# Optimization experiments

Measured on AMD Instinct MI355X. Metric: run time of the kernel, lower is better.

## Reference

```python
import jax, jax.numpy as jnp
import numpy as np

N = 10000      # nodes
E = 160000     # edges (before self-loops)
F_IN = 128     # num_features
H1, D1 = 4, 256   # conv1: 4 heads x 256, concat -> 1024
D2 = 256          # conv2: 1 head x 256
NEG_SLOPE = 0.2


def setup_inputs() -> dict:
    key = jax.random.key(0)
    ks = jax.random.split(key, 12)
    def p(k, shape, fan):
        return jax.random.normal(k, shape, jnp.float32) / np.float32(np.sqrt(fan))
    return {
        "x": jax.random.normal(ks[0], (N, F_IN), jnp.float32),
        "edge_index": jax.random.randint(ks[1], (2, E), 0, N, jnp.int32),
        "W1": p(ks[2], (F_IN, H1 * D1), F_IN),
        "att_src1": p(ks[3], (H1, D1), D1),
        "att_dst1": p(ks[4], (H1, D1), D1),
        "b1": jnp.zeros((H1 * D1,), jnp.float32),
        "lin1_W": p(ks[5], (F_IN, H1 * D1), F_IN),
        "lin1_b": jnp.zeros((H1 * D1,), jnp.float32),
        "W2": p(ks[6], (H1 * D1, D2), H1 * D1),
        "att_src2": p(ks[7], (1, D2), D2),
        "att_dst2": p(ks[8], (1, D2), D2),
        "b2": jnp.zeros((D2,), jnp.float32),
        "lin2_W": p(ks[9], (H1 * D1, D2), H1 * D1),
        "lin2_b": jnp.zeros((D2,), jnp.float32),
    }


def gat_layer(x, src, dst, W, a_src, a_dst, b, heads, d):
    """PyG-style GATConv: transform, edgewise LeakyReLU attention,
    segment-softmax over destination neighborhoods, scatter-add, concat heads."""
    n = x.shape[0]
    h = (x @ W).reshape(n, heads, d)                       # [N, H, D]
    s_src = jnp.einsum('nhd,hd->nh', h, a_src)             # per-node scores
    s_dst = jnp.einsum('nhd,hd->nh', h, a_dst)
    e = jax.nn.leaky_relu(s_src[src] + s_dst[dst], NEG_SLOPE)   # [E, H]
    m = jax.ops.segment_max(e, dst, num_segments=n)        # stable softmax per dst
    p = jnp.exp(e - m[dst])
    z = jax.ops.segment_sum(p, dst, num_segments=n)
    alpha = p / (z[dst] + 1e-16)                           # [E, H]
    msg = h[src] * alpha[:, :, None]                       # [E, H, D]
    out = jax.ops.segment_sum(msg, dst, num_segments=n)    # [N, H, D]
    return out.reshape(n, heads * d) + b, alpha


def reference(x, edge_index, W1, att_src1, att_dst1, b1, lin1_W, lin1_b,
              W2, att_src2, att_dst2, b2, lin2_W, lin2_b):
    n = x.shape[0]
    loop = jnp.arange(n, dtype=edge_index.dtype)           # add self-loops (PyG default)
    src = jnp.concatenate([edge_index[0], loop])
    dst = jnp.concatenate([edge_index[1], loop])
    h1, alpha1 = gat_layer(x, src, dst, W1, att_src1, att_dst1, b1, H1, D1)
    h1 = jax.nn.elu(h1 + x @ lin1_W + lin1_b)              # conv1 + lin1 residual, ELU
    h2, _ = gat_layer(h1, src, dst, W2, att_src2, att_dst2, b2, 1, D2)
    out = h2 + h1 @ lin2_W + lin2_b                        # conv2 + lin2 residual
    return out, alpha1
```

## Files before the change

kernel.cpp:

```cpp
#include <hip/hip_runtime.h>
#include <hip/hip_bf16.h>
#include <math.h>

#define NN   10000
#define EE   160000
#define ETOT 170000
#define FIN  128
#define C1   1024
#define NH1  4
#define D1   256
#define D2   256
#define MAXD 96

typedef __attribute__((ext_vector_type(8))) short bf16x8;
typedef __attribute__((ext_vector_type(4))) float f32x4;

__device__ __forceinline__ float b2f(unsigned short u)
{
    union { unsigned int i; float f; } c; c.i = (unsigned int)u << 16; return c.f;
}
__device__ __forceinline__ unsigned short f2b(float x)
{
    return __builtin_bit_cast(unsigned short, __float2bfloat16(x));
}
__device__ __forceinline__ void split1(float x, unsigned short &h, unsigned short &l)
{
    __hip_bfloat16 hb = __float2bfloat16(x);
    float r = x - __bfloat162float(hb);
    h = __builtin_bit_cast(unsigned short, hb);
    l = __builtin_bit_cast(unsigned short, __float2bfloat16(r));
}

__global__ __launch_bounds__(256)
void split_A(const float* __restrict__ X, unsigned short* __restrict__ A2, int M, int K)
{
    int idx = blockIdx.x * 256 + threadIdx.x;
    int kq4 = K >> 2;
    if (idx >= M * kq4) return;
    int m = idx / kq4, kq = idx % kq4;
    float4 v = *(const float4*)&X[(size_t)m * K + kq * 4];
    ushort4 h, l;
    split1(v.x, h.x, l.x); split1(v.y, h.y, l.y);
    split1(v.z, h.z, l.z); split1(v.w, h.w, l.w);
    unsigned short* row = A2 + (size_t)m * (2 * K);
    *(ushort4*)&row[kq * 4]     = h;
    *(ushort4*)&row[K + kq * 4] = l;
}

__global__ __launch_bounds__(256)
void split_Bt(const float* __restrict__ B0, const float* __restrict__ B1,
              int K, int N0, int Ntot, unsigned short* __restrict__ Bt)
{
    int idx = blockIdx.x * 256 + threadIdx.x;
    int total = Ntot * (K >> 2);
    if (idx >= total) return;
    int n = idx % Ntot;
    int kq = idx / Ntot;
    int k = kq * 4;
    const float* B; int nc, nb;
    if (n < N0) { B = B0; nc = n; nb = N0; }
    else        { B = B1; nc = n - N0; nb = Ntot - N0; }
    float v0 = B[(size_t)(k + 0) * nb + nc];
    float v1 = B[(size_t)(k + 1) * nb + nc];
    float v2 = B[(size_t)(k + 2) * nb + nc];
    float v3 = B[(size_t)(k + 3) * nb + nc];
    ushort4 h, l;
    split1(v0, h.x, l.x); split1(v1, h.y, l.y);
    split1(v2, h.z, l.z); split1(v3, h.w, l.w);
    unsigned short* row = Bt + (size_t)n * (3 * K);
    *(ushort4*)&row[k]         = h;
    *(ushort4*)&row[K + k]     = h;
    *(ushort4*)&row[2 * K + k] = l;
}

__device__ __forceinline__ void glds16(const void* g, void* l)
{
    __builtin_amdgcn_global_load_lds((const __attribute__((address_space(1))) void*)g,
                                     (__attribute__((address_space(3))) void*)l, 16, 0, 0);
}

template<int BN, int WM, int WN, int BK>
__global__ __launch_bounds__(256)
void gemm_split(const unsigned short* __restrict__ A, int lda, int ka2,
                const unsigned short* __restrict__ Bt, int keff,
                unsigned short* __restrict__ outPb, float* __restrict__ outR,
                int M, int nsplit, int ldR, int ntn,
                const float* __restrict__ bias0, const float* __restrict__ bias1)
{
    constexpr int BM   = 128;
    constexpr int WTM  = BM / WM,  WTN = BN / WN;
    constexpr int FJ   = WTM / 16, FI  = WTN / 16;
    constexpr int KS   = BK / 32;
    constexpr int SLOTS = BK / 8;
    constexpr int SMASK = SLOTS - 1;
    constexpr int SWSH  = (BK == 32) ? 1 : 0;
    constexpr int RPC  = 512 / BK;
    constexpr int ACH  = BM / RPC;
    constexpr int NCH  = (BM + BN) / RPC;
    constexpr int CPW  = NCH / 4;
    constexpr int ABUF = BM * BK, BBUF = BN * BK;

    __shared__ __align__(16) unsigned short sA[2 * ABUF];
    __shared__ __align__(16) unsigned short sB[2 * BBUF];

    const int tid = threadIdx.x;
    const int w = tid >> 6, lane = tid & 63;

    const int cpx = gridDim.x >> 3;
    const int t0  = (blockIdx.x & 7) * cpx + (blockIdx.x >> 3);
    const int m0 = (t0 / ntn) * BM;
    const int n0 = (t0 % ntn) * BN;
    const int wm = w / WN, wn = w % WN;

    f32x4 acc[FI][FJ] = {};

    const unsigned short* gp[CPW];
    int lofs[CPW];
    bool isa[CPW];
    {
        const int r  = lane / SLOTS;
        const int sl = lane % SLOTS;
        const int ssl = sl ^ ((r >> SWSH) & SMASK);
        #pragma unroll
        for (int cc = 0; cc < CPW; ++cc) {
            int c = w * CPW + cc;
            if (c < ACH) {
                int gm = m0 + c * RPC + r; if (gm >= M) gm = M - 1;
                gp[cc]   = A + (size_t)gm * lda + ssl * 8;
                lofs[cc] = c * 512;
                isa[cc]  = true;
            } else {
                int gn = n0 + (c - ACH) * RPC + r;
                gp[cc]   = Bt + (size_t)gn * keff + ssl * 8;
                lofs[cc] = (c - ACH) * 512;
                isa[cc]  = false;
            }
        }
    }

    const int rAl = wm * WTM + (lane & 15);
    const int rBl = wn * WTN + (lane & 15);
    const int koff = (lane >> 4) * 8;
    const int nit = keff / BK;
    int cur = 0;

    #pragma unroll
    for (int cc = 0; cc < CPW; ++cc)
        glds16(gp[cc], (isa[cc] ? sA : sB) + lofs[cc]);
    __syncthreads();

    for (int it = 0; it < nit; ++it) {
        if (it + 1 < nit) {
            int kn = (it + 1) * BK;
            int kAn = (kn >= ka2) ? (kn - ka2) : kn;
            #pragma unroll
            for (int cc = 0; cc < CPW; ++cc) {
                unsigned short* dst = (isa[cc] ? sA + (cur ^ 1) * ABUF
                                               : sB + (cur ^ 1) * BBUF) + lofs[cc];
                glds16(gp[cc] + (isa[cc] ? kAn : kn), dst);
            }
        }
        const unsigned short* cA = sA + cur * ABUF;
        const unsigned short* cB = sB + cur * BBUF;
        #pragma unroll
        for (int ks = 0; ks < KS; ++ks) {
            const int sIdx = (ks * 32 + koff) >> 3;
            bf16x8 av[FJ], bv[FI];
            #pragma unroll
            for (int f = 0; f < FI; ++f) {
                int row = rBl + f * 16;
                bv[f] = *(const bf16x8*)&cB[row * BK + ((sIdx ^ ((row >> SWSH) & SMASK)) << 3)];
            }
            #pragma unroll
            for (int f = 0; f < FJ; ++f) {
                int row = rAl + f * 16;
                av[f] = *(const bf16x8*)&cA[row * BK + ((sIdx ^ ((row >> SWSH) & SMASK)) << 3)];
            }
            #pragma unroll
            for (int fj = 0; fj < FJ; ++fj)
                #pragma unroll
                for (int fi = 0; fi < FI; ++fi)
                    acc[fi][fj] = __builtin_amdgcn_mfma_f32_16x16x32_bf16(
                        bv[fi], av[fj], acc[fi][fj], 0, 0, 0);
        }
        __syncthreads();
        cur ^= 1;
    }

    const int lrow = lane & 15;
    const int lcol = (lane >> 4) << 2;
    #pragma unroll
    for (int fj = 0; fj < FJ; ++fj) {
        int row = m0 + wm * WTM + fj * 16 + lrow;
        if (row >= M) continue;
        #pragma unroll
        for (int fi = 0; fi < FI; ++fi) {
            int col = n0 + wn * WTN + fi * 16 + lcol;
            f32x4 v = acc[fi][fj];
            if (col < nsplit) {
                ushort4 o;
                o.x = f2b(v[0]); o.y = f2b(v[1]); o.z = f2b(v[2]); o.w = f2b(v[3]);
                *(ushort4*)&outPb[(size_t)row * nsplit + col] = o;
            } else {
                int c = col - nsplit;
                const float4 g0 = *(const float4*)&bias0[c];
                const float4 g1 = *(const float4*)&bias1[c];
                v[0] += g0.x + g1.x; v[1] += g0.y + g1.y;
                v[2] += g0.z + g1.z; v[3] += g0.w + g1.w;
                *(f32x4*)&outR[(size_t)row * ldR + c] = v;
            }
        }
    }
}

__global__ __launch_bounds__(256)
void scores_h4(const unsigned short* __restrict__ h, const float* __restrict__ a_src,
               const float* __restrict__ a_dst, float* __restrict__ s_src,
               float* __restrict__ s_dst)
{
    const int n = blockIdx.x;
    const int w = threadIdx.x >> 6;
    const int lane = threadIdx.x & 63;
    ushort4 u = *(const ushort4*)&h[(size_t)n * C1 + w * D1 + lane * 4];
    float4 as = ((const float4*)&a_src[w * D1])[lane];
    float4 ad = ((const float4*)&a_dst[w * D1])[lane];
    float vx = b2f(u.x), vy = b2f(u.y), vz = b2f(u.z), vw = b2f(u.w);
    float ss = vx * as.x + vy * as.y + vz * as.z + vw * as.w;
    float sd = vx * ad.x + vy * ad.y + vz * ad.z + vw * ad.w;
    #pragma unroll
    for (int off = 32; off; off >>= 1) {
        ss += __shfl_xor(ss, off);
        sd += __shfl_xor(sd, off);
    }
    if (lane == 0) { s_src[n * NH1 + w] = ss; s_dst[n * NH1 + w] = sd; }
}

__global__ __launch_bounds__(256)
void scores_h1(const unsigned short* __restrict__ h, const float* __restrict__ a_src,
               const float* __restrict__ a_dst, float* __restrict__ s_src,
               float* __restrict__ s_dst)
{
    const int n = blockIdx.x * 4 + (threadIdx.x >> 6);
    if (n >= NN) return;
    const int lane = threadIdx.x & 63;
    ushort4 u = *(const ushort4*)&h[(size_t)n * D2 + lane * 4];
    float4 as = ((const float4*)a_src)[lane];
    float4 ad = ((const float4*)a_dst)[lane];
    float vx = b2f(u.x), vy = b2f(u.y), vz = b2f(u.z), vw = b2f(u.w);
    float ss = vx * as.x + vy * as.y + vz * as.z + vw * as.w;
    float sd = vx * ad.x + vy * ad.y + vz * ad.z + vw * ad.w;
    #pragma unroll
    for (int off = 32; off; off >>= 1) {
        ss += __shfl_xor(ss, off);
        sd += __shfl_xor(sd, off);
    }
    if (lane == 0) { s_src[n] = ss; s_dst[n] = sd; }
}

__global__ void count_deg(const int* __restrict__ dstp, int* __restrict__ cnt)
{
    int e = blockIdx.x * 256 + threadIdx.x;
    if (e >= ETOT) return;
    int d = (e < EE) ? dstp[e] : (e - EE);
    atomicAdd(&cnt[d], 1);
}

__global__ __launch_bounds__(1024)
void scan_kernel(const int* __restrict__ cnt, int* __restrict__ row_ptr)
{
    __shared__ int part[1024];
    const int t = threadIdx.x;
    int local[10];
    int s = 0;
    #pragma unroll
    for (int j = 0; j < 10; ++j) {
        int idx = t * 10 + j;
        local[j] = s;
        s += (idx < NN) ? cnt[idx] : 0;
    }
    part[t] = s;
    __syncthreads();
    for (int off = 1; off < 1024; off <<= 1) {
        int v = (t >= off) ? part[t - off] : 0;
        __syncthreads();
        part[t] += v;
        __syncthreads();
    }
    int prefix = (t > 0) ? part[t - 1] : 0;
    #pragma unroll
    for (int j = 0; j < 10; ++j) {
        int idx = t * 10 + j;
        if (idx < NN) row_ptr[idx] = prefix + local[j];
    }
    if (t == 0) row_ptr[NN] = ETOT;
}

__global__ void scatter_edges(const int* __restrict__ srcp, const int* __restrict__ dstp,
                              const int* __restrict__ row_ptr, int* __restrict__ fill,
                              int* __restrict__ csr_src, int* __restrict__ csr_eid)
{
    int e = blockIdx.x * 256 + threadIdx.x;
    if (e >= ETOT) return;
    int s, d;
    if (e < EE) { s = srcp[e]; d = dstp[e]; } else { s = d = e - EE; }
    int pos = row_ptr[d] + atomicAdd(&fill[d], 1);
    csr_src[pos] = s;
    csr_eid[pos] = e;
}

__global__ __launch_bounds__(256)
void aggregate1(const unsigned short* __restrict__ h1b, const float* __restrict__ s_src,
                const float* __restrict__ s_dst,
                const int* __restrict__ row_ptr, const int* __restrict__ csr_src,
                const int* __restrict__ csr_eid, const float* __restrict__ base_in,
                unsigned short* __restrict__ a2stk, float* __restrict__ alpha_out)
{
    __shared__ float lalpha[NH1][MAXD];
    const int n = blockIdx.x;
    const int t = threadIdx.x;
    const int h = t >> 6;
    const int lane = t & 63;
    const int start = row_ptr[n], end = row_ptr[n + 1];
    const float sd = s_dst[n * NH1 + h];

    float m = -1e30f;
    for (int i = start + lane; i < end; i += 64) {
        float sc = s_src[csr_src[i] * NH1 + h] + sd;
        sc = sc > 0.f ? sc : 0.2f * sc;
        m = fmaxf(m, sc);
    }
    #pragma unroll
    for (int off = 32; off; off >>= 1) m = fmaxf(m, __shfl_xor(m, off));
    float z = 0.f;
    for (int i = start + lane; i < end; i += 64) {
        float sc = s_src[csr_src[i] * NH1 + h] + sd;
        sc = sc > 0.f ? sc : 0.2f * sc;
        z += __expf(sc - m);
    }
    #pragma unroll
    for (int off = 32; off; off >>= 1) z += __shfl_xor(z, off);
    const float invz = 1.f / (z + 1e-16f);
    for (int i = start + lane; i < end; i += 64) {
        float sc = s_src[csr_src[i] * NH1 + h] + sd;
        sc = sc > 0.f ? sc : 0.2f * sc;
        float a = __expf(sc - m) * invz;
        alpha_out[(size_t)csr_eid[i] * NH1 + h] = a;
        int idx = i - start;
        if (idx < MAXD) lalpha[h][idx] = a;
    }
    __syncthreads();

    float4 base = *(const float4*)&base_in[(size_t)n * C1 + t * 4];
    float4 acc = make_float4(0.f, 0.f, 0.f, 0.f);
    for (int i = start; i < end; ++i) {
        const int s = csr_src[i];
        const int idx = i - start;
        float a;
        if (idx < MAXD) {
            a = lalpha[h][idx];
        } else {
            float sc = s_src[s * NH1 + h] + sd;
            sc = sc > 0.f ? sc : 0.2f * sc;
            a = __expf(sc - m) * invz;
        }
        ushort4 v = *(const ushort4*)&h1b[(size_t)s * C1 + t * 4];
        acc.x += a * b2f(v.x); acc.y += a * b2f(v.y);
        acc.z += a * b2f(v.z); acc.w += a * b2f(v.w);
    }
    float4 r;
    r.x = acc.x + base.x; r.y = acc.y + base.y;
    r.z = acc.z + base.z; r.w = acc.w + base.w;
    r.x = r.x > 0.f ? r.x : expm1f(r.x);
    r.y = r.y > 0.f ? r.y : expm1f(r.y);
    r.z = r.z > 0.f ? r.z : expm1f(r.z);
    r.w = r.w > 0.f ? r.w : expm1f(r.w);
    __syncthreads();
    ushort4 hi, lo;
    split1(r.x, hi.x, lo.x); split1(r.y, hi.y, lo.y);
    split1(r.z, hi.z, lo.z); split1(r.w, hi.w, lo.w);
    unsigned short* row = a2stk + (size_t)n * (2 * C1);
    *(ushort4*)&row[t * 4]      = hi;
    *(ushort4*)&row[C1 + t * 4] = lo;
}

__global__ __launch_bounds__(64)
void aggregate2(const unsigned short* __restrict__ h2b, const float* __restrict__ s_src,
                const float* __restrict__ s_dst,
                const int* __restrict__ row_ptr, const int* __restrict__ csr_src,
                const float* __restrict__ accin, float* __restrict__ out)
{
    __shared__ float lalpha[MAXD];
    const int n = blockIdx.x;
    const int t = threadIdx.x;
    const int start = row_ptr[n], end = row_ptr[n + 1];
    const float sd = s_dst[n];

    float m = -1e30f;
    for (int i = start + t; i < end; i += 64) {
        float sc = s_src[csr_src[i]] + sd;
        sc = sc > 0.f ? sc : 0.2f * sc;
        m = fmaxf(m, sc);
    }
    #pragma unroll
    for (int off = 32; off; off >>= 1) m = fmaxf(m, __shfl_xor(m, off));
    float z = 0.f;
    for (int i = start + t; i < end; i += 64) {
        float sc = s_src[csr_src[i]] + sd;
        sc = sc > 0.f ? sc : 0.2f * sc;
        z += __expf(sc - m);
    }
    #pragma unroll
    for (int off = 32; off; off >>= 1) z += __shfl_xor(z, off);
    const float invz = 1.f / (z + 1e-16f);
    for (int i = start + t; i < end; i += 64) {
        float sc = s_src[csr_src[i]] + sd;
        sc = sc > 0.f ? sc : 0.2f * sc;
        int idx = i - start;
        if (idx < MAXD) lalpha[idx] = __expf(sc - m) * invz;
    }
    __syncthreads();

    float4 acc = make_float4(0.f, 0.f, 0.f, 0.f);
    for (int i = start; i < end; ++i) {
        const int s = csr_src[i];
        const int idx = i - start;
        float a;
        if (idx < MAXD) {
            a = lalpha[idx];
        } else {
            float sc = s_src[s] + sd;
            sc = sc > 0.f ? sc : 0.2f * sc;
            a = __expf(sc - m) * invz;
        }
        ushort4 v = *(const ushort4*)&h2b[(size_t)s * D2 + t * 4];
        acc.x += a * b2f(v.x); acc.y += a * b2f(v.y);
        acc.z += a * b2f(v.z); acc.w += a * b2f(v.w);
    }
    float4 base = *(const float4*)&accin[(size_t)n * D2 + t * 4];
    float4 r;
    r.x = acc.x + base.x; r.y = acc.y + base.y;
    r.z = acc.z + base.z; r.w = acc.w + base.w;
    *(float4*)&out[(size_t)n * D2 + t * 4] = r;
}

extern "C" void kernel_launch(void* const* d_in, const int* in_sizes, int n_in,
                              void* d_out, int out_size, void* d_ws, size_t ws_size,
                              hipStream_t stream)
{
    const float* x        = (const float*)d_in[0];
    const int*   ei       = (const int*)  d_in[1];
    const float* W1       = (const float*)d_in[2];
    const float* att_src1 = (const float*)d_in[3];
    const float* att_dst1 = (const float*)d_in[4];
    const float* b1       = (const float*)d_in[5];
    const float* lin1_W   = (const float*)d_in[6];
    const float* lin1_b   = (const float*)d_in[7];
    const float* W2       = (const float*)d_in[8];
    const float* att_src2 = (const float*)d_in[9];
    const float* att_dst2 = (const float*)d_in[10];
    const float* b2       = (const float*)d_in[11];
    const float* lin2_W   = (const float*)d_in[12];
    const float* lin2_b   = (const float*)d_in[13];
    const int* srcp = ei;
    const int* dstp = ei + EE;

    float* out    = (float*)d_out;
    float* alpha1 = out + (size_t)NN * D2;

    float* fw = (float*)d_ws;
    float* acc1   = fw;   fw += (size_t)NN * C1;
    unsigned short* h1b = (unsigned short*)fw; fw += (size_t)NN * C1 / 2;
    unsigned short* h2b = (unsigned short*)fw; fw += (size_t)NN * D2 / 2;
    float* acc2   = fw;   fw += (size_t)NN * D2;
    unsigned short* A1stk = (unsigned short*)fw; fw += (size_t)NN * FIN;
    unsigned short* Bt1   = (unsigned short*)fw; fw += (size_t)2048 * 3 * FIN / 2;
    unsigned short* Bt2   = (unsigned short*)fw; fw += (size_t)512 * 3 * C1 / 2;
    float* s_src1 = fw;   fw += NN * NH1;
    float* s_dst1 = fw;   fw += NN * NH1;
    float* s_src2 = fw;   fw += NN;
    float* s_dst2 = fw;   fw += NN;
    int* ip      = (int*)fw;
    int* cnt     = ip;    ip += NN;
    int* fill    = ip;    ip += NN;
    int* row_ptr = ip;    ip += NN + 4;
    int* csr_src = ip;    ip += ETOT;
    int* csr_eid = ip;    ip += ETOT;

    unsigned short* A2stk = (unsigned short*)acc1;

    hipMemsetAsync(cnt, 0, 2 * NN * sizeof(int), stream);

    const int mt = (NN + 127) / 128;

    split_A<<<(NN * (FIN / 4) + 255) / 256, 256, 0, stream>>>(x, A1stk, NN, FIN);
    split_Bt<<<(2048 * (FIN / 4) + 255) / 256, 256, 0, stream>>>(W1, lin1_W, FIN, C1, 2048, Bt1);
    gemm_split<128, 2, 2, 32><<<mt * 16, 256, 0, stream>>>(
        A1stk, 2 * FIN, 2 * FIN, Bt1, 3 * FIN, h1b, acc1, NN, C1, C1, 16, lin1_b, b1);
    scores_h4<<<NN, 256, 0, stream>>>(h1b, att_src1, att_dst1, s_src1, s_dst1);

    count_deg<<<(ETOT + 255) / 256, 256, 0, stream>>>(dstp, cnt);
    scan_kernel<<<1, 1024, 0, stream>>>(cnt, row_ptr);
    scatter_edges<<<(ETOT + 255) / 256, 256, 0, stream>>>(srcp, dstp, row_ptr, fill,
                                                          csr_src, csr_eid);

    aggregate1<<<NN, 256, 0, stream>>>(h1b, s_src1, s_dst1, row_ptr, csr_src, csr_eid,
                                       acc1, A2stk, alpha1);

    split_Bt<<<(512 * (C1 / 4) + 255) / 256, 256, 0, stream>>>(W2, lin2_W, C1, D2, 512, Bt2);
    gemm_split<64, 4, 1, 64><<<mt * 8, 256, 0, stream>>>(
        A2stk, 2 * C1, 2 * C1, Bt2, 3 * C1, h2b, acc2, NN, D2, D2, 8, lin2_b, b2);

    scores_h1<<<(NN + 3) / 4, 256, 0, stream>>>(h2b, att_src2, att_dst2, s_src2, s_dst2);
    aggregate2<<<NN, 64, 0, stream>>>(h2b, s_src2, s_dst2, row_ptr, csr_src, acc2, out);
}
```

Measured before the change: 237.4 us.

## Fuse prep kernels into one launch and sort CSR segments by source

Merges split_A, both split_Bt weight conversions and the degree count into a single prep kernel with block-range dispatch, removing three kernel launches. Adds a sort_segments kernel that bitonic-sorts each destination's neighbor list by (src, eid) within a wavefront, making the atomic-order CSR deterministic and improving gather locality in aggregation. The trade-off is one extra kernel launch and the sort work, and segments with more than 64 neighbors are left unsorted.

```diff
diff --git a/kernel.cpp b/kernel.cpp
--- a/kernel.cpp
+++ b/kernel.cpp
@@ -31,10 +31,10 @@
     l = __builtin_bit_cast(unsigned short, __float2bfloat16(r));
 }
 
-__global__ __launch_bounds__(256)
-void split_A(const float* __restrict__ X, unsigned short* __restrict__ A2, int M, int K)
-{
-    int idx = blockIdx.x * 256 + threadIdx.x;
+__device__ __forceinline__ void split_A_body(const float* __restrict__ X,
+                                             unsigned short* __restrict__ A2,
+                                             int M, int K, int idx)
+{
     int kq4 = K >> 2;
     if (idx >= M * kq4) return;
     int m = idx / kq4, kq = idx % kq4;
@@ -47,11 +47,11 @@
     *(ushort4*)&row[K + kq * 4] = l;
 }
 
-__global__ __launch_bounds__(256)
-void split_Bt(const float* __restrict__ B0, const float* __restrict__ B1,
-              int K, int N0, int Ntot, unsigned short* __restrict__ Bt)
-{
-    int idx = blockIdx.x * 256 + threadIdx.x;
+__device__ __forceinline__ void split_Bt_body(const float* __restrict__ B0,
+                                              const float* __restrict__ B1,
+                                              int K, int N0, int Ntot,
+                                              unsigned short* __restrict__ Bt, int idx)
+{
     int total = Ntot * (K >> 2);
     if (idx >= total) return;
     int n = idx % Ntot;
@@ -71,6 +71,30 @@
     *(ushort4*)&row[k]         = h;
     *(ushort4*)&row[K + k]     = h;
     *(ushort4*)&row[2 * K + k] = l;
+}
+
+__global__ __launch_bounds__(256)
+void prep(const float* __restrict__ x, unsigned short* __restrict__ A1stk,
+          const float* __restrict__ W1, const float* __restrict__ lin1_W,
+          unsigned short* __restrict__ Bt1,
+          const float* __restrict__ W2, const float* __restrict__ lin2_W,
+          unsigned short* __restrict__ Bt2,
+          const int* __restrict__ dstp, int* __restrict__ cnt)
+{
+    const int b = blockIdx.x, t = threadIdx.x;
+    if (b < 1250) {
+        split_A_body(x, A1stk, NN, FIN, b * 256 + t);
+    } else if (b < 1506) {
+        split_Bt_body(W1, lin1_W, FIN, C1, 2048, Bt1, (b - 1250) * 256 + t);
+    } else if (b < 2018) {
+        split_Bt_body(W2, lin2_W, C1, D2, 512, Bt2, (b - 1506) * 256 + t);
+    } else {
+        int e = (b - 2018) * 256 + t;
+        if (e < ETOT) {
+            int d = (e < EE) ? dstp[e] : (e - EE);
+            atomicAdd(&cnt[d], 1);
+        }
+    }
 }
 
 __device__ __forceinline__ void glds16(const void* g, void* l)
@@ -257,14 +281,6 @@
     if (lane == 0) { s_src[n] = ss; s_dst[n] = sd; }
 }
 
-__global__ void count_deg(const int* __restrict__ dstp, int* __restrict__ cnt)
-{
-    int e = blockIdx.x * 256 + threadIdx.x;
-    if (e >= ETOT) return;
-    int d = (e < EE) ? dstp[e] : (e - EE);
-    atomicAdd(&cnt[d], 1);
-}
-
 __global__ __launch_bounds__(1024)
 void scan_kernel(const int* __restrict__ cnt, int* __restrict__ row_ptr)
 {
@@ -306,6 +322,34 @@
     int pos = row_ptr[d] + atomicAdd(&fill[d], 1);
     csr_src[pos] = s;
     csr_eid[pos] = e;
+}
+
+__global__ __launch_bounds__(256)
+void sort_segments(const int* __restrict__ row_ptr, int* __restrict__ csr_src,
+                   int* __restrict__ csr_eid)
+{
+    const int n = blockIdx.x * 4 + (threadIdx.x >> 6);
+    if (n >= NN) return;
+    const int lane = threadIdx.x & 63;
+    const int start = row_ptr[n], end = row_ptr[n + 1];
+    const int deg = end - start;
+    if (deg > 64) return;
+    unsigned int key = 0xFFFFFFFFu;
+    if (lane < deg)
+        key = ((unsigned)csr_src[start + lane] << 18) | (unsigned)csr_eid[start + lane];
+    #pragma unroll
+    for (int k = 2; k <= 64; k <<= 1) {
+        #pragma unroll
+        for (int j = k >> 1; j > 0; j >>= 1) {
+            unsigned int pk = (unsigned int)__shfl_xor((int)key, j);
+            bool wantMin = (((lane & k) == 0) == ((lane & j) == 0));
+            key = wantMin ? (key < pk ? key : pk) : (key > pk ? key : pk);
+        }
+    }
+    if (lane < deg) {
+        csr_src[start + lane] = (int)(key >> 18);
+        csr_eid[start + lane] = (int)(key & 0x3FFFFu);
+    }
 }
 
 __global__ __launch_bounds__(256)
@@ -492,21 +536,20 @@
 
     const int mt = (NN + 127) / 128;
 
-    split_A<<<(NN * (FIN / 4) + 255) / 256, 256, 0, stream>>>(x, A1stk, NN, FIN);
-    split_Bt<<<(2048 * (FIN / 4) + 255) / 256, 256, 0, stream>>>(W1, lin1_W, FIN, C1, 2048, Bt1);
+    prep<<<2683, 256, 0, stream>>>(x, A1stk, W1, lin1_W, Bt1, W2, lin2_W, Bt2, dstp, cnt);
+
+    scan_kernel<<<1, 1024, 0, stream>>>(cnt, row_ptr);
+    scatter_edges<<<(ETOT + 255) / 256, 256, 0, stream>>>(srcp, dstp, row_ptr, fill,
+                                                          csr_src, csr_eid);
+    sort_segments<<<(NN + 3) / 4, 256, 0, stream>>>(row_ptr, csr_src, csr_eid);
+
     gemm_split<128, 2, 2, 32><<<mt * 16, 256, 0, stream>>>(
         A1stk, 2 * FIN, 2 * FIN, Bt1, 3 * FIN, h1b, acc1, NN, C1, C1, 16, lin1_b, b1);
     scores_h4<<<NN, 256, 0, stream>>>(h1b, att_src1, att_dst1, s_src1, s_dst1);
 
-    count_deg<<<(ETOT + 255) / 256, 256, 0, stream>>>(dstp, cnt);
-    scan_kernel<<<1, 1024, 0, stream>>>(cnt, row_ptr);
-    scatter_edges<<<(ETOT + 255) / 256, 256, 0, stream>>>(srcp, dstp, row_ptr, fill,
-                                                          csr_src, csr_eid);
-
     aggregate1<<<NN, 256, 0, stream>>>(h1b, s_src1, s_dst1, row_ptr, csr_src, csr_eid,
                                        acc1, A2stk, alpha1);
 
-    split_Bt<<<(512 * (C1 / 4) + 255) / 256, 256, 0, stream>>>(W2, lin2_W, C1, D2, 512, Bt2);
     gemm_split<64, 4, 1, 64><<<mt * 8, 256, 0, stream>>>(
         A2stk, 2 * C1, 2 * C1, Bt2, 3 * C1, h2b, acc2, NN, D2, D2, 8, lin2_b, b2);
 
```

After: 236.9 us. No clear change (-0.2%).
